# Kernel optimization log

Measured on AMD Instinct MI355X. Metric: run time of the kernel, lower is better.

Reference implementation:

```python
import jax, jax.numpy as jnp
import numpy as np

B, N, D, H, A = 1024, 8, 256, 512, 4  # batch, num_objects, embedding_dim, hidden_dim, action_dim


def _edge_list(batch, n):
    # Fully connected (no self-loops) over n nodes, replicated per sample with offset b*n.
    pairs = np.array([(i, j) for i in range(n) for j in range(n) if i != j], dtype=np.int32)
    off = (np.arange(batch, dtype=np.int32) * n)[:, None]
    row = (pairs[:, 0][None, :] + off).reshape(-1)
    col = (pairs[:, 1][None, :] + off).reshape(-1)
    return jnp.asarray(row), jnp.asarray(col)


def _layer_norm(x, g, b):
    m = x.mean(-1, keepdims=True)
    v = x.var(-1, keepdims=True)
    return (x - m) / jnp.sqrt(v + 1e-5) * g + b


def _mlp(x, w1, b1, w2, b2, g, bn, w3, b3):
    h = jax.nn.relu(x @ w1 + b1)
    h = jax.nn.relu(_layer_norm(h @ w2 + b2, g, bn))
    return h @ w3 + b3


def setup_inputs() -> dict:
    key = jax.random.key(0)
    ks = jax.random.split(key, 12)
    def w(k, shape):
        return jax.random.normal(k, shape, jnp.float32) / np.sqrt(shape[0]).astype(np.float32)
    return {
        "states": jax.random.normal(ks[0], (B, N, D), jnp.float32),
        "action": jax.random.randint(ks[1], (B,), 0, A),
        # edge MLP: 3D -> H -> H (LN) -> H
        "e_w1": w(ks[2], (3 * D, H)), "e_b1": jnp.zeros((H,), jnp.float32),
        "e_w2": w(ks[3], (H, H)),     "e_b2": jnp.zeros((H,), jnp.float32),
        "e_g":  jnp.ones((H,), jnp.float32), "e_bn": jnp.zeros((H,), jnp.float32),
        "e_w3": w(ks[4], (H, H)),     "e_b3": jnp.zeros((H,), jnp.float32),
        # node MLP: H + D + A -> H -> H (LN) -> D
        "n_w1": w(ks[5], (H + D + A, H)), "n_b1": jnp.zeros((H,), jnp.float32),
        "n_w2": w(ks[6], (H, H)),         "n_b2": jnp.zeros((H,), jnp.float32),
        "n_g":  jnp.ones((H,), jnp.float32), "n_bn": jnp.zeros((H,), jnp.float32),
        "n_w3": w(ks[7], (H, D)),         "n_b3": jnp.zeros((D,), jnp.float32),
    }


def reference(states, action,
              e_w1, e_b1, e_w2, e_b2, e_g, e_bn, e_w3, e_b3,
              n_w1, n_b1, n_w2, n_b2, n_g, n_bn, n_w3, n_b3):
    eP = (e_w1, e_b1, e_w2, e_b2, e_g, e_bn, e_w3, e_b3)
    nP = (n_w1, n_b1, n_w2, n_b2, n_g, n_bn, n_w3, n_b3)
    flat = states.reshape(-1, D)                       # [B*N, D]
    row, col = _edge_list(B, N - 1)                    # faithful: edge list over N-1 objects
    E = row.shape[0]
    # copy_action / embodied: one-hot action repeated per object
    av = jnp.repeat(jax.nn.one_hot(action, A, dtype=flat.dtype), N, axis=0)  # [B*N, A]
    # round 0: edge_attr starts as zeros like node features
    e = _mlp(jnp.concatenate([flat[row], jnp.zeros((E, D), flat.dtype), flat[col]], 1), *eP)
    agg = jax.ops.segment_sum(e, row, num_segments=B * N)  # [B*N, H]
    node = _mlp(jnp.concatenate([flat, av, agg], 1), *nP)   # [B*N, D]
    flat = flat + node
    av0 = jnp.zeros_like(av)
    for _ in range(N - 1):
        e = _mlp(jnp.concatenate([flat[row], node[row], flat[col]], 1), *eP)
        agg = jax.ops.segment_sum(e, row, num_segments=B * N)
        node = _mlp(jnp.concatenate([flat, av0, agg], 1), *nP)
        flat = flat + node
    return flat.reshape(B, N, D)
```

## Files before the change

kernel.cpp:

```cpp
#include <hip/hip_runtime.h>
#include <cstddef>

typedef _Float16 f16x8 __attribute__((ext_vector_type(8)));
typedef _Float16 f16x4 __attribute__((ext_vector_type(4)));
typedef float f32x16 __attribute__((ext_vector_type(16)));
typedef unsigned short ushort_t;

#define NSEG 7168
#define NNODE 8192

enum { EP_NONE = 0, EP_BIAS = 1, EP_RAWP = 2, EP_NL1 = 3, EP_NL3 = 4 };

#define PHASE_BARRIER() do { asm volatile("s_waitcnt lgkmcnt(0)" ::: "memory"); \
                             __builtin_amdgcn_s_barrier(); } while (0)

#define RELU8(v) do { _Pragma("unroll") \
  for (int j_ = 0; j_ < 8; ++j_) v[j_] = v[j_] > (_Float16)0 ? v[j_] : (_Float16)0; } while (0)

__global__ __launch_bounds__(256)
void prepack(const float* __restrict__ W, ushort_t* __restrict__ P,
             int koff, int kcnt, int Nsrc, int NTpack, int noff) {
  int idx = blockIdx.x * 256 + threadIdx.x;
  if (idx >= kcnt * Nsrc) return;
  int kl = idx / Nsrc, n = idx - kl * Nsrc + noff;
  _Float16 h = (_Float16)W[idx];
  int k = koff + kl;
  size_t o = ((((size_t)(k >> 4)) * NTpack + (n >> 5)) * 64 + ((k >> 3) & 1) * 32 + (n & 31)) * 8 + (k & 7);
  P[o] = __builtin_bit_cast(ushort_t, h);
}

__global__ __launch_bounds__(256)
void v6k(const float* __restrict__ eb3, const float* __restrict__ nw1,
         float* __restrict__ v6) {
  int n = blockIdx.x * 256 + threadIdx.x;
  if (n >= 512) return;
  float a = 0.f;
  for (int k = 0; k < 512; ++k) a += eb3[k] * nw1[(size_t)(260 + k) * 512 + n];
  v6[n] = 6.f * a;
}

template <int NCOLB, int EPI, int EDGE, int LNIN, int X1F16, int OUTF16>
__global__ __launch_bounds__(256, 4)
void gemmT(const void* __restrict__ X1v, int ld1, int nph1,
           const void* __restrict__ X2v, int ld2, int nph2,
           const ushort_t* __restrict__ Sm, const ushort_t* __restrict__ Tm,
           const ushort_t* __restrict__ P,
           const float* __restrict__ bias, const float* __restrict__ bias2,
           const int* __restrict__ action, const float* __restrict__ wact,
           const float* __restrict__ lnpart,
           const float* __restrict__ lng, const float* __restrict__ lnbn,
           void* __restrict__ Yv, float* __restrict__ Yres,
           float* __restrict__ Part, int m0base) {
  constexpr int N = NCOLB * 128;
  constexpr int NT = N / 32;
  const int u = threadIdx.x;
  const int nwg = gridDim.x;
  const int qq = nwg >> 3, r8 = nwg & 7;
  const int xcd = blockIdx.x & 7, inx = blockIdx.x >> 3;
  const int logical = (xcd < r8 ? xcd * (qq + 1) : r8 * (qq + 1) + (xcd - r8) * qq) + inx;
  const int mY = (logical / NCOLB) * 64;
  const int cb = logical - (logical / NCOLB) * NCOLB;
  const int nB = cb * 128;
  const int lane = u & 63, w = u >> 6;
  const int wr = w >> 1, wc = w & 1;
  const int r31 = lane & 31, rt2 = lane >> 5;

  __shared__ ushort_t lA[16384];

  const int kcA = w * 2, kcB = w * 2 + 1;
  const int widx0 = (((rt2 * 8 + kcA) * 2 + 0) * 32 + (r31 ^ ((kcA & 3) << 3))) * 8;
  const int widx1 = (((rt2 * 8 + kcA) * 2 + 1) * 32 + (r31 ^ ((kcA & 3) << 3))) * 8;
  const int widx2 = (((rt2 * 8 + kcB) * 2 + 0) * 32 + (r31 ^ ((kcB & 3) << 3))) * 8;
  const int widx3 = (((rt2 * 8 + kcB) * 2 + 1) * 32 + (r31 ^ ((kcB & 3) << 3))) * 8;

  const ushort_t* sB = nullptr;
  const ushort_t* tB = nullptr;
  const float* x1f = nullptr;
  const ushort_t* x1h = nullptr;
  const ushort_t* x2h = nullptr;
  if (EDGE) {
    int e = m0base + mY + lane;
    int b = e / 42, p = e - b * 42;
    int i = p / 6, tt = p - i * 6;
    int j = tt + (tt >= i ? 1 : 0);
    sB = Sm + (size_t)(b * 7 + i) * 1024 + w * 32;
    tB = Tm + (size_t)(b * 7 + j) * 1024 + w * 32;
  } else {
    if (X1F16) x1h = (const ushort_t*)X1v + (size_t)(mY + lane) * ld1 + w * 32;
    else       x1f = (const float*)X1v + (size_t)(mY + lane) * ld1 + w * 32;
    if (nph2 > 0) x2h = (const ushort_t*)X2v + (size_t)(mY + lane) * ld2 + w * 32;
  }
  float mym = 0.f, myr = 0.f;
  if (LNIN) {
    const float* pp = lnpart + (size_t)(mY + lane) * 16;
    float S_ = 0.f, Q_ = 0.f;
    #pragma unroll
    for (int i = 0; i < 8; ++i) { S_ += pp[i]; Q_ += pp[8 + i]; }
    mym = S_ * (1.f / 512.f);
    myr = rsqrtf(Q_ * (1.f / 512.f) - mym * mym + 1e-5f);
  }

  f16x8 xc0, xc1, xc2, xc3;
  auto loadx = [&](int ph) {
    if (EDGE) {
      const ushort_t* sp = sB + ph * 128;
      const ushort_t* tp = tB + ph * 128;
      f16x8 s0 = *(const f16x8*)sp,        t0 = *(const f16x8*)tp;
      f16x8 s1 = *(const f16x8*)(sp + 8),  t1 = *(const f16x8*)(tp + 8);
      f16x8 s2 = *(const f16x8*)(sp + 16), t2 = *(const f16x8*)(tp + 16);
      f16x8 s3 = *(const f16x8*)(sp + 24), t3 = *(const f16x8*)(tp + 24);
      xc0 = s0 + t0; xc1 = s1 + t1; xc2 = s2 + t2; xc3 = s3 + t3;
      RELU8(xc0); RELU8(xc1); RELU8(xc2); RELU8(xc3);
    } else if (!X1F16 && ph < nph1) {
      const float* src = x1f + ph * 128;
      float4 l0 = *(const float4*)(src +  0), h0 = *(const float4*)(src +  4);
      float4 l1 = *(const float4*)(src +  8), h1 = *(const float4*)(src + 12);
      float4 l2 = *(const float4*)(src + 16), h2 = *(const float4*)(src + 20);
      float4 l3 = *(const float4*)(src + 24), h3 = *(const float4*)(src + 28);
#define CVT8(X, lo, hi) do { X[0]=(_Float16)lo.x; X[1]=(_Float16)lo.y; \
      X[2]=(_Float16)lo.z; X[3]=(_Float16)lo.w; X[4]=(_Float16)hi.x; \
      X[5]=(_Float16)hi.y; X[6]=(_Float16)hi.z; X[7]=(_Float16)hi.w; } while (0)
      CVT8(xc0, l0, h0); CVT8(xc1, l1, h1); CVT8(xc2, l2, h2); CVT8(xc3, l3, h3);
#undef CVT8
    } else {
      const ushort_t* src = (ph < nph1) ? x1h + ph * 128 : x2h + (ph - nph1) * 128;
      xc0 = *(const f16x8*)src;
      xc1 = *(const f16x8*)(src + 8);
      xc2 = *(const f16x8*)(src + 16);
      xc3 = *(const f16x8*)(src + 24);
      if (LNIN) {
        const int kb = ph * 128 + w * 32;
#define LN8(X, OFS) do { _Pragma("unroll") for (int j_ = 0; j_ < 8; ++j_) { \
        float xx = (float)X[j_]; \
        xx = fmaxf((xx - mym) * myr * lng[kb + (OFS) + j_] + lnbn[kb + (OFS) + j_], 0.f); \
        X[j_] = (_Float16)xx; } } while (0)
        LN8(xc0, 0); LN8(xc1, 8); LN8(xc2, 16); LN8(xc3, 24);
#undef LN8
      }
    }
  };
  auto cvtwrite = [&](int b) {
    const int base = b * 8192;
    *(f16x8*)&lA[base + widx0] = xc0;
    *(f16x8*)&lA[base + widx1] = xc1;
    *(f16x8*)&lA[base + widx2] = xc2;
    *(f16x8*)&lA[base + widx3] = xc3;
  };

  f32x16 acc0, acc1;
  #pragma unroll
  for (int q = 0; q < 16; ++q) { acc0[q] = 0.f; acc1[q] = 0.f; }

  const int nph = nph1 + nph2;
  const int ntb = (nB >> 5) + wc * 2;
  const int TOT = nph * 8;

#define LOADA(S, A_) do { \
    const int aofs_ = lbase + (((wr * 8 + (S)) * 2 + rt2) * 32 + (r31 ^ (((S) & 3) << 3))) * 8; \
    A_ = *(const f16x8*)&lA[aofs_]; } while (0)

#define LOADB(G_, H0, H1) do { \
    const ushort_t* bp_ = P + (((size_t)(G_) * NT + ntb) * 64 + lane) * 8; \
    H0 = *(const f16x8*)bp_; \
    H1 = *(const f16x8*)(bp_ + 512); } while (0)

#define MFMA2(AH, H0, H1) do { \
    acc0 = __builtin_amdgcn_mfma_f32_32x32x16_f16(AH, H0, acc0, 0, 0, 0); \
    acc1 = __builtin_amdgcn_mfma_f32_32x32x16_f16(AH, H1, acc1, 0, 0, 0); } while (0)

  loadx(0);
  cvtwrite(0);
  if (nph > 1) loadx(1);
  PHASE_BARRIER();
  f16x8 b00, b01, b10, b11, b20, b21, b30, b31;
  LOADB(0, b00, b01);
  LOADB(1, b10, b11);
  LOADB(2, b20, b21);
  LOADB(3, b30, b31);

  #pragma unroll 1
  for (int ph = 0; ph < nph; ++ph) {
    if (ph + 1 < nph) {
      cvtwrite((ph + 1) & 1);
      if (ph + 2 < nph) loadx(ph + 2);
    }
    const int lbase = (ph & 1) * 8192;
    const int g0 = ph * 8;
    f16x8 ac, an;
    LOADA(0, ac);
#define STEP(S, BH, BL) do { \
    if ((S) < 7) LOADA((S) + 1, an); \
    f16x8 h0 = BH, h1 = BL; \
    if (g0 + (S) + 4 < TOT) LOADB(g0 + (S) + 4, BH, BL); \
    MFMA2(ac, h0, h1); \
    if ((S) < 7) ac = an; } while (0)
    STEP(0, b00, b01);
    STEP(1, b10, b11);
    STEP(2, b20, b21);
    STEP(3, b30, b31);
    STEP(4, b00, b01);
    STEP(5, b10, b11);
    STEP(6, b20, b21);
    STEP(7, b30, b31);
#undef STEP
    if (ph + 1 < nph) PHASE_BARRIER();
  }

  const int col0 = nB + wc * 64 + r31;
  float v[2][16];
  {
    float bc0 = (EPI == EP_NONE) ? 0.f : bias[col0];
    float bc1 = (EPI == EP_NONE) ? 0.f : bias[col0 + 32];
    #pragma unroll
    for (int q = 0; q < 16; ++q) {
      v[0][q] = acc0[q] + bc0;
      v[1][q] = acc1[q] + bc1;
    }
  }

  if (EPI == EP_NL1) {
    #pragma unroll
    for (int q = 0; q < 16; ++q) {
      int m = mY + wr * 32 + (q & 3) + 8 * (q >> 2) + 4 * rt2;
      if (m < NSEG) {
        v[0][q] += bias2[col0];
        v[1][q] += bias2[col0 + 32];
      }
      if (action != nullptr) {
        const float* wrp = wact + (size_t)(256 + action[m >> 3]) * 512;
        v[0][q] += wrp[col0];
        v[1][q] += wrp[col0 + 32];
      }
    }
    #pragma unroll
    for (int ct = 0; ct < 2; ++ct)
      #pragma unroll
      for (int q = 0; q < 16; ++q) v[ct][q] = fmaxf(v[ct][q], 0.f);
  }

  if (EPI == EP_RAWP) {
    float sv[16], qv[16];
    #pragma unroll
    for (int q = 0; q < 16; ++q) {
      sv[q] = v[0][q] + v[1][q];
      qv[q] = v[0][q] * v[0][q] + v[1][q] * v[1][q];
    }
    #pragma unroll
    for (int mm = 1; mm <= 16; mm <<= 1) {
      #pragma unroll
      for (int q = 0; q < 16; ++q) {
        sv[q] += __shfl_xor(sv[q], mm);
        qv[q] += __shfl_xor(qv[q], mm);
      }
    }
    if (r31 == 0) {
      #pragma unroll
      for (int q = 0; q < 16; ++q) {
        int m = mY + wr * 32 + (q & 3) + 8 * (q >> 2) + 4 * rt2;
        Part[(size_t)m * 16 + cb * 2 + wc] = sv[q];
        Part[(size_t)m * 16 + 8 + cb * 2 + wc] = qv[q];
      }
    }
  }

  #pragma unroll
  for (int ct = 0; ct < 2; ++ct) {
    #pragma unroll
    for (int q = 0; q < 16; ++q) {
      int m = mY + wr * 32 + (q & 3) + 8 * (q >> 2) + 4 * rt2;
      float z = v[ct][q];
      if (OUTF16)
        ((ushort_t*)Yv)[(size_t)m * N + col0 + ct * 32] =
            __builtin_bit_cast(ushort_t, (_Float16)z);
      else
        ((float*)Yv)[(size_t)m * N + col0 + ct * 32] = z;
      if (EPI == EP_NL3) Yres[(size_t)m * N + col0 + ct * 32] += z;
    }
  }
#undef LOADA
#undef LOADB
#undef MFMA2
}

__global__ __launch_bounds__(256)
void h2_sum_ln(const ushort_t* __restrict__ H2, const float* __restrict__ Part,
               const float* __restrict__ g, const float* __restrict__ bn,
               ushort_t* __restrict__ SS) {
  __shared__ float smu[12], srs[12];
  const int u = threadIdx.x;
  const int g2 = blockIdx.x * 2;
  if (u < 12) {
    const float* pp = Part + ((size_t)g2 * 6 + u) * 16;
    float S = 0.f, Q = 0.f;
    #pragma unroll
    for (int i = 0; i < 8; ++i) { S += pp[i]; Q += pp[8 + i]; }
    float m = S * (1.f / 512.f);
    smu[u] = m;
    srs[u] = rsqrtf(Q * (1.f / 512.f) - m * m + 1e-5f);
  }
  __syncthreads();
  const int ln = g2 + (u >> 7);
  const int lloc = (u >> 7) * 6;
  const int c4 = (u & 127) * 4;
  float4 gv = *(const float4*)(g + c4);
  float4 bv = *(const float4*)(bn + c4);
  float a0 = 0.f, a1 = 0.f, a2 = 0.f, a3 = 0.f;
  #pragma unroll
  for (int r = 0; r < 6; ++r) {
    int row = ln * 6 + r;
    f16x4 y = *(const f16x4*)(H2 + (size_t)row * 512 + c4);
    float m = smu[lloc + r], rs = srs[lloc + r];
    a0 += fmaxf(((float)y[0] - m) * rs * gv.x + bv.x, 0.f);
    a1 += fmaxf(((float)y[1] - m) * rs * gv.y + bv.y, 0.f);
    a2 += fmaxf(((float)y[2] - m) * rs * gv.z + bv.z, 0.f);
    a3 += fmaxf(((float)y[3] - m) * rs * gv.w + bv.w, 0.f);
  }
  f16x4 o;
  o[0] = (_Float16)a0; o[1] = (_Float16)a1; o[2] = (_Float16)a2; o[3] = (_Float16)a3;
  *(f16x4*)(SS + (size_t)ln * 512 + c4) = o;
}

extern "C" void kernel_launch(void* const* d_in, const int* in_sizes, int n_in,
                              void* d_out, int out_size, void* d_ws, size_t ws_size,
                              hipStream_t stream) {
  (void)in_sizes; (void)n_in; (void)out_size;
  const float* states = (const float*)d_in[0];
  const int* action = (const int*)d_in[1];
  const float* e_w1 = (const float*)d_in[2];
  const float* e_b1 = (const float*)d_in[3];
  const float* e_w2 = (const float*)d_in[4];
  const float* e_b2 = (const float*)d_in[5];
  const float* e_g = (const float*)d_in[6];
  const float* e_bn = (const float*)d_in[7];
  const float* e_w3 = (const float*)d_in[8];
  const float* e_b3 = (const float*)d_in[9];
  const float* n_w1 = (const float*)d_in[10];
  const float* n_b1 = (const float*)d_in[11];
  const float* n_w2 = (const float*)d_in[12];
  const float* n_b2 = (const float*)d_in[13];
  const float* n_g = (const float*)d_in[14];
  const float* n_bn = (const float*)d_in[15];
  const float* n_w3 = (const float*)d_in[16];
  const float* n_b3 = (const float*)d_in[17];

  float* flat = (float*)d_out;
  float* fp = (float*)d_ws;
  float* Mbuf = fp;  fp += 262144;
  float* v6 = fp;    fp += 512;
  float* b1ext = fp; fp += 1024;
  float* PartE = fp; fp += 688128;
  float* PartN = fp; fp += 131072;
  ushort_t* us = (ushort_t*)fp;
  ushort_t* node = us; us += 2097152;
  ushort_t* SS = us;   us += 4194304;
  ushort_t* G = us;    us += 4194304;
  ushort_t* G2 = us;   us += 4194304;
  ushort_t* STb = us;  us += 7340032;
  ushort_t* PeST = us; us += 524288;
  ushort_t* PeW2 = us; us += 262144;
  ushort_t* Ptmp = us; us += 262144;
  ushort_t* PnW1M = us; us += 393216;
  ushort_t* PnW2 = us;  us += 262144;
  ushort_t* PnW3 = us;  us += 131072;
  ushort_t* H2 = us;

  const size_t fixedB = (size_t)((char*)H2 - (char*)d_ws);
  int nc = 32;
  for (int cand = 1; cand <= 32; cand <<= 1)
    if (fixedB + (43008ull / cand) * 512ull * 2ull <= ws_size) { nc = cand; break; }
  const int spc = 1024 / nc;
  const int epc = spc * 42;

  hipMemsetAsync(PeST, 0, 524288 * 2, stream);
  prepack<<<1024, 256, 0, stream>>>(e_w1, PeST, 0, 512, 512, 32, 0);
  prepack<<<512, 256, 0, stream>>>(e_w1 + 262144, PeST, 0, 256, 512, 32, 512);
  prepack<<<1024, 256, 0, stream>>>(e_w2, PeW2, 0, 512, 512, 16, 0);
  prepack<<<1024, 256, 0, stream>>>(n_w1 + 133120, Ptmp, 0, 512, 512, 16, 0);
  prepack<<<512, 256, 0, stream>>>(n_w1, PnW1M, 0, 256, 512, 16, 0);
  prepack<<<1024, 256, 0, stream>>>(n_w2, PnW2, 0, 512, 512, 16, 0);
  prepack<<<512, 256, 0, stream>>>(n_w3, PnW3, 0, 512, 256, 8, 0);
  hipMemcpyAsync(b1ext, e_b1, 512 * 4, hipMemcpyDeviceToDevice, stream);
  hipMemsetAsync(b1ext + 512, 0, 512 * 4, stream);
  gemmT<4, EP_NONE, 0, 0, 0, 0><<<32, 256, 0, stream>>>(
      e_w3, 512, 4, nullptr, 0, 0, nullptr, nullptr, Ptmp, nullptr, nullptr,
      nullptr, nullptr, nullptr, nullptr, nullptr, Mbuf, nullptr, nullptr, 0);
  prepack<<<1024, 256, 0, stream>>>(Mbuf, PnW1M, 256, 512, 512, 16, 0);
  v6k<<<2, 256, 0, stream>>>(e_b3, n_w1, v6);
  hipMemsetAsync(SS + (size_t)NSEG * 512, 0, (size_t)(NNODE - NSEG) * 512 * 2, stream);
  hipMemcpyAsync(flat, states, (size_t)NNODE * 256 * 4, hipMemcpyDeviceToDevice, stream);

  for (int round = 0; round < 8; ++round) {
    if (round == 0)
      gemmT<8, EP_BIAS, 0, 0, 0, 1><<<896, 256, 0, stream>>>(
          flat, 256, 2, nullptr, 0, 0, nullptr, nullptr, PeST, b1ext, nullptr,
          nullptr, nullptr, nullptr, nullptr, nullptr, STb, nullptr, nullptr, 0);
    else
      gemmT<8, EP_BIAS, 0, 0, 0, 1><<<896, 256, 0, stream>>>(
          flat, 256, 2, node, 256, 2, nullptr, nullptr, PeST, b1ext, nullptr,
          nullptr, nullptr, nullptr, nullptr, nullptr, STb, nullptr, nullptr, 0);
    for (int ch = 0; ch < nc; ++ch) {
      gemmT<4, EP_RAWP, 1, 0, 0, 1><<<(epc / 64) * 4, 256, 0, stream>>>(
          nullptr, 0, 4, nullptr, 0, 0, STb, STb + 512, PeW2, e_b2, nullptr,
          nullptr, nullptr, nullptr, nullptr, nullptr,
          H2, nullptr, PartE, ch * epc);
      h2_sum_ln<<<(spc * 7) / 2, 256, 0, stream>>>(
          H2, PartE, e_g, e_bn, SS + (size_t)ch * spc * 7 * 512);
    }
    gemmT<4, EP_NL1, 0, 0, 0, 1><<<512, 256, 0, stream>>>(
        flat, 256, 2, SS, 512, 4, nullptr, nullptr, PnW1M, n_b1, v6,
        (round == 0) ? action : nullptr, n_w1,
        nullptr, nullptr, nullptr, G, nullptr, nullptr, 0);
    gemmT<4, EP_RAWP, 0, 0, 1, 1><<<512, 256, 0, stream>>>(
        G, 512, 4, nullptr, 0, 0, nullptr, nullptr, PnW2, n_b2, nullptr,
        nullptr, nullptr, nullptr, nullptr, nullptr, G2, nullptr, PartN, 0);
    gemmT<2, EP_NL3, 0, 1, 1, 1><<<256, 256, 0, stream>>>(
        G2, 512, 4, nullptr, 0, 0, nullptr, nullptr, PnW3, n_b3, nullptr,
        nullptr, nullptr, PartN, n_g, n_bn, node, flat, nullptr, 0);
  }
}
```

Before: 1.282 ms.

## Add dedicated wide-tile edge layer-2 GEMM kernel with fused LN partial sums

```diff
diff --git a/kernel.cpp b/kernel.cpp
--- a/kernel.cpp
+++ b/kernel.cpp
@@ -16,6 +16,8 @@
 
 #define RELU8(v) do { _Pragma("unroll") \
   for (int j_ = 0; j_ < 8; ++j_) v[j_] = v[j_] > (_Float16)0 ? v[j_] : (_Float16)0; } while (0)
+
+#define MF(a, b, c) __builtin_amdgcn_mfma_f32_32x32x16_f16(a, b, c, 0, 0, 0)
 
 __global__ __launch_bounds__(256)
 void prepack(const float* __restrict__ W, ushort_t* __restrict__ P,
@@ -165,8 +167,8 @@
     H1 = *(const f16x8*)(bp_ + 512); } while (0)
 
 #define MFMA2(AH, H0, H1) do { \
-    acc0 = __builtin_amdgcn_mfma_f32_32x32x16_f16(AH, H0, acc0, 0, 0, 0); \
-    acc1 = __builtin_amdgcn_mfma_f32_32x32x16_f16(AH, H1, acc1, 0, 0, 0); } while (0)
+    acc0 = MF(AH, H0, acc0); \
+    acc1 = MF(AH, H1, acc1); } while (0)
 
   loadx(0);
   cvtwrite(0);
@@ -280,6 +282,153 @@
 #undef LOADA
 #undef LOADB
 #undef MFMA2
+}
+
+__global__ __launch_bounds__(512, 4)
+void edgeW(const ushort_t* __restrict__ Sm, const ushort_t* __restrict__ Tm,
+           const ushort_t* __restrict__ P, const float* __restrict__ bias,
+           ushort_t* __restrict__ H2, float* __restrict__ Part, int m0base) {
+  const int u = threadIdx.x;
+  const int nwg = gridDim.x;
+  const int qq = nwg >> 3, r8 = nwg & 7;
+  const int xcd = blockIdx.x & 7, inx = blockIdx.x >> 3;
+  const int logical = (xcd < r8 ? xcd * (qq + 1) : r8 * (qq + 1) + (xcd - r8) * qq) + inx;
+  const int mY = logical * 64;
+  const int lane = u & 63, w = u >> 6;
+  const int wrh = w >> 2, wcq = w & 3;
+  const int r31 = lane & 31, rt2 = lane >> 5;
+
+  __shared__ ushort_t lA[16384];
+
+  const int widx0 = (((rt2 * 8 + w) * 2 + 0) * 32 + (r31 ^ ((w & 3) << 3))) * 8;
+
+  int e = m0base + mY + lane;
+  int b = e / 42, p = e - b * 42;
+  int ii = p / 6, tt = p - ii * 6;
+  int jj = tt + (tt >= ii ? 1 : 0);
+  const ushort_t* sA = Sm + (size_t)(b * 7 + ii) * 1024 + w * 16;
+  const ushort_t* tA = Tm + (size_t)(b * 7 + jj) * 1024 + w * 16;
+
+  f16x8 xc0, xc1;
+  auto loadx = [&](int ph) {
+    const ushort_t* sp = sA + ph * 128;
+    const ushort_t* tp = tA + ph * 128;
+    f16x8 s0 = *(const f16x8*)sp, t0 = *(const f16x8*)tp;
+    f16x8 s1 = *(const f16x8*)(sp + 8), t1 = *(const f16x8*)(tp + 8);
+    xc0 = s0 + t0; xc1 = s1 + t1;
+    RELU8(xc0); RELU8(xc1);
+  };
+  auto cvtwrite = [&](int bb) {
+    *(f16x8*)&lA[bb * 8192 + widx0] = xc0;
+    *(f16x8*)&lA[bb * 8192 + widx0 + 256] = xc1;
+  };
+
+  f32x16 acc0, acc1, acc2, acc3;
+  #pragma unroll
+  for (int q = 0; q < 16; ++q) { acc0[q] = 0.f; acc1[q] = 0.f; acc2[q] = 0.f; acc3[q] = 0.f; }
+
+  const int tb0 = wcq * 4;
+
+#define LOADA(S_, A_) do { \
+    const int aofs_ = lbase + (((wrh * 8 + (S_)) * 2 + rt2) * 32 + (r31 ^ (((S_) & 3) << 3))) * 8; \
+    A_ = *(const f16x8*)&lA[aofs_]; } while (0)
+
+#define LOADB4(G_, B0, B1, B2, B3) do { \
+    const ushort_t* bp_ = P + (((size_t)(G_) * 16 + tb0) * 64 + lane) * 8; \
+    B0 = *(const f16x8*)bp_;          B1 = *(const f16x8*)(bp_ + 512); \
+    B2 = *(const f16x8*)(bp_ + 1024); B3 = *(const f16x8*)(bp_ + 1536); } while (0)
+
+  loadx(0);
+  cvtwrite(0);
+  loadx(1);
+  PHASE_BARRIER();
+  f16x8 be0, be1, be2, be3, bo0, bo1, bo2, bo3;
+  LOADB4(0, be0, be1, be2, be3);
+  LOADB4(1, bo0, bo1, bo2, bo3);
+
+  #pragma unroll 1
+  for (int ph = 0; ph < 4; ++ph) {
+    if (ph + 1 < 4) {
+      cvtwrite((ph + 1) & 1);
+      if (ph + 2 < 4) loadx(ph + 2);
+    }
+    const int lbase = (ph & 1) * 8192;
+    const int g0 = ph * 8;
+    f16x8 ac, an;
+    LOADA(0, ac);
+#define STEPE(S_) do { \
+    if ((S_) < 7) LOADA((S_) + 1, an); \
+    acc0 = MF(ac, be0, acc0); acc1 = MF(ac, be1, acc1); \
+    acc2 = MF(ac, be2, acc2); acc3 = MF(ac, be3, acc3); \
+    if (g0 + (S_) + 2 < 32) LOADB4(g0 + (S_) + 2, be0, be1, be2, be3); \
+    if ((S_) < 7) ac = an; } while (0)
+#define STEPO(S_) do { \
+    if ((S_) < 7) LOADA((S_) + 1, an); \
+    acc0 = MF(ac, bo0, acc0); acc1 = MF(ac, bo1, acc1); \
+    acc2 = MF(ac, bo2, acc2); acc3 = MF(ac, bo3, acc3); \
+    if (g0 + (S_) + 2 < 32) LOADB4(g0 + (S_) + 2, bo0, bo1, bo2, bo3); \
+    if ((S_) < 7) ac = an; } while (0)
+    STEPE(0); STEPO(1); STEPE(2); STEPO(3);
+    STEPE(4); STEPO(5); STEPE(6); STEPO(7);
+#undef STEPE
+#undef STEPO
+    if (ph + 1 < 4) PHASE_BARRIER();
+  }
+#undef LOADA
+#undef LOADB4
+
+  const int colb = wcq * 128 + r31;
+  float v0[16], v1[16], v2[16], v3[16];
+  {
+    float bc0 = bias[colb], bc1 = bias[colb + 32];
+    float bc2 = bias[colb + 64], bc3 = bias[colb + 96];
+    #pragma unroll
+    for (int q = 0; q < 16; ++q) {
+      v0[q] = acc0[q] + bc0;
+      v1[q] = acc1[q] + bc1;
+      v2[q] = acc2[q] + bc2;
+      v3[q] = acc3[q] + bc3;
+    }
+  }
+  {
+    float sa[16], qa[16], sb[16], qb[16];
+    #pragma unroll
+    for (int q = 0; q < 16; ++q) {
+      sa[q] = v0[q] + v1[q];
+      qa[q] = v0[q] * v0[q] + v1[q] * v1[q];
+      sb[q] = v2[q] + v3[q];
+      qb[q] = v2[q] * v2[q] + v3[q] * v3[q];
+    }
+    #pragma unroll
+    for (int mm = 1; mm <= 16; mm <<= 1) {
+      #pragma unroll
+      for (int q = 0; q < 16; ++q) {
+        sa[q] += __shfl_xor(sa[q], mm);
+        qa[q] += __shfl_xor(qa[q], mm);
+        sb[q] += __shfl_xor(sb[q], mm);
+        qb[q] += __shfl_xor(qb[q], mm);
+      }
+    }
+    if (r31 == 0) {
+      #pragma unroll
+      for (int q = 0; q < 16; ++q) {
+        int m = mY + wrh * 32 + (q & 3) + 8 * (q >> 2) + 4 * rt2;
+        Part[(size_t)m * 16 + wcq * 2 + 0] = sa[q];
+        Part[(size_t)m * 16 + wcq * 2 + 1] = sb[q];
+        Part[(size_t)m * 16 + 8 + wcq * 2 + 0] = qa[q];
+        Part[(size_t)m * 16 + 8 + wcq * 2 + 1] = qb[q];
+      }
+    }
+  }
+  #pragma unroll
+  for (int q = 0; q < 16; ++q) {
+    int m = mY + wrh * 32 + (q & 3) + 8 * (q >> 2) + 4 * rt2;
+    ushort_t* dst = H2 + (size_t)m * 512 + colb;
+    dst[0]  = __builtin_bit_cast(ushort_t, (_Float16)v0[q]);
+    dst[32] = __builtin_bit_cast(ushort_t, (_Float16)v1[q]);
+    dst[64] = __builtin_bit_cast(ushort_t, (_Float16)v2[q]);
+    dst[96] = __builtin_bit_cast(ushort_t, (_Float16)v3[q]);
+  }
 }
 
 __global__ __launch_bounds__(256)
@@ -399,10 +548,8 @@
           flat, 256, 2, node, 256, 2, nullptr, nullptr, PeST, b1ext, nullptr,
           nullptr, nullptr, nullptr, nullptr, nullptr, STb, nullptr, nullptr, 0);
     for (int ch = 0; ch < nc; ++ch) {
-      gemmT<4, EP_RAWP, 1, 0, 0, 1><<<(epc / 64) * 4, 256, 0, stream>>>(
-          nullptr, 0, 4, nullptr, 0, 0, STb, STb + 512, PeW2, e_b2, nullptr,
-          nullptr, nullptr, nullptr, nullptr, nullptr,
-          H2, nullptr, PartE, ch * epc);
+      edgeW<<<epc / 64, 512, 0, stream>>>(
+          STb, STb + 512, PeW2, e_b2, H2, PartE, ch * epc);
       h2_sum_ln<<<(spc * 7) / 2, 256, 0, stream>>>(
           H2, PartE, e_g, e_bn, SS + (size_t)ch * spc * 7 * 512);
     }
```

Result: slower. 1.533 ms (+19.6%).
